# Optimization experiments

Hardware: AMD Instinct MI355X
Metric: run time of the kernel (lower is better)

Reference implementation:

```python
import jax, jax.numpy as jnp
import numpy as np


def setup_inputs() -> dict:
    key = jax.random.key(0)
    k1, k2, k3, k4 = jax.random.split(key, 4)
    B, N, d, E = 4, 768, 16, 12288
    emb_nodes = jax.random.normal(k1, (B, N, d), dtype=jnp.float32)
    edges = jax.random.randint(k2, (B, 2, E), 0, N, dtype=jnp.int64)
    # nn.Linear(2*d, 1): weight [1, 2d], bias [1]
    W = jax.random.normal(k3, (2 * d,), dtype=jnp.float32) * 0.1
    b = jax.random.normal(k4, (1,), dtype=jnp.float32) * 0.1
    return {"emb_nodes": emb_nodes, "edges": edges, "W": W, "b": b}


def reference(emb_nodes, edges, W, b):
    B, N, d = emb_nodes.shape
    # all-pairs (i, j): i = repeat_interleave, j = tile  -> [B, N*N, d]
    inter = jnp.repeat(emb_nodes, N, axis=1)
    rep = jnp.tile(emb_nodes, (1, N, 1))
    # original detaches the pair embeddings before the decoder
    edge_embeddings = jax.lax.stop_gradient(jnp.concatenate([inter, rep], axis=-1))  # [B, N*N, 2d]
    logits = edge_embeddings @ W + b[0]  # [B, N*N]
    # self-loop detection via embedding equality (|e_i - e_j| sum == 0)
    non_empty = jnp.abs(inter - rep).sum(axis=-1) != 0
    logits = jnp.where(non_empty, logits, jnp.float32(-10.0))
    # ground-truth edge indicator: scatter 1 at flat index i*N + j
    flat = edges[:, 0] * N + edges[:, 1]  # [B, E]
    truth = jnp.zeros((B, N * N), dtype=emb_nodes.dtype)
    truth = truth.at[jnp.arange(B)[:, None], flat].set(1.0)
    return (edge_embeddings, logits, truth)
```

## Files before the change

### kernel.cpp

```cpp
#include <hip/hip_runtime.h>

constexpr int B = 4;
constexpr int N = 768;
constexpr int D = 16;
constexpr int E = 12288;
constexpr int NN = N * N;
constexpr int PAIRS = B * NN;
constexpr long long EE_FLOATS = (long long)PAIRS * 2 * D;

__device__ __forceinline__ float dot4(float4 a, float4 b) {
    return a.x * b.x + a.y * b.y + a.z * b.z + a.w * b.w;
}
__device__ __forceinline__ float absdiff4(float4 a, float4 b) {
    return fabsf(a.x - b.x) + fabsf(a.y - b.y) + fabsf(a.z - b.z) + fabsf(a.w - b.w);
}

__global__ __launch_bounds__(256) void row_fused_kernel(
    const float4* __restrict__ emb4, const float* __restrict__ W,
    const float* __restrict__ bias, float4* __restrict__ ee4,
    float* __restrict__ logits, float* __restrict__ truth) {
    const int row = blockIdx.x;
    const int b = row / N;
    const int i = row - b * N;
    const float4* __restrict__ eb = emb4 + (size_t)b * N * 4;
    const float4* __restrict__ ei = eb + i * 4;

    const int t = threadIdx.x;
    const int q = t & 7;
    const int qq = q & 3;
    const bool isI = (q < 4);
    const float4 eiq = ei[qq];

    float4* __restrict__ orow = ee4 + (size_t)row * (N * 8);
#pragma unroll
    for (int k = 0; k < (N * 8) / 256; ++k) {
        const int f = t + k * 256;
        float4 v = eiq;
        if (!isI) v = eb[(f >> 3) * 4 + qq];
        orow[f] = v;
    }

    const float4* __restrict__ W4 = (const float4*)W;
    const float4 wa0 = W4[0], wa1 = W4[1], wa2 = W4[2], wa3 = W4[3];
    const float4 wb0 = W4[4], wb1 = W4[5], wb2 = W4[6], wb3 = W4[7];
    const float4 e0 = ei[0], e1 = ei[1], e2 = ei[2], e3 = ei[3];
    const float base =
        dot4(e0, wa0) + dot4(e1, wa1) + dot4(e2, wa2) + dot4(e3, wa3) + bias[0];
    float* __restrict__ lrow = logits + (size_t)row * N;
    float* __restrict__ trow = truth + (size_t)row * N;
#pragma unroll
    for (int k = 0; k < N / 256; ++k) {
        const int j = t + k * 256;
        const float4* __restrict__ ej = eb + j * 4;
        const float4 c0 = ej[0], c1 = ej[1], c2 = ej[2], c3 = ej[3];
        const float acc = base + dot4(c0, wb0) + dot4(c1, wb1) +
                          dot4(c2, wb2) + dot4(c3, wb3);
        const float diff = absdiff4(e0, c0) + absdiff4(e1, c1) +
                           absdiff4(e2, c2) + absdiff4(e3, c3);
        lrow[j] = (diff != 0.f) ? acc : -10.0f;
        trow[j] = 0.0f;
    }
}

__global__ void truth_scatter_kernel(const int* __restrict__ edges,
                                     float* __restrict__ truth) {
    int tid = blockIdx.x * blockDim.x + threadIdx.x;
    if (tid >= B * E) return;
    int b = tid / E;
    int e = tid - b * E;
    int src = edges[b * 2 * E + e];
    int dst = edges[b * 2 * E + E + e];
    truth[(size_t)b * NN + src * N + dst] = 1.0f;
}

extern "C" void kernel_launch(void* const* d_in, const int* in_sizes, int n_in,
                              void* d_out, int out_size, void* d_ws, size_t ws_size,
                              hipStream_t stream) {
    const float4* emb4 = (const float4*)d_in[0];
    const int* edges = (const int*)d_in[1];
    const float* W = (const float*)d_in[2];
    const float* bias = (const float*)d_in[3];

    float* out = (float*)d_out;
    float* ee = out;
    float* logits = out + EE_FLOATS;
    float* truth = out + EE_FLOATS + (long long)PAIRS;

    row_fused_kernel<<<B * N, 256, 0, stream>>>(emb4, W, bias, (float4*)ee,
                                                logits, truth);
    truth_scatter_kernel<<<(B * E + 255) / 256, 256, 0, stream>>>(edges, truth);
}
```

Measured before the change: 335.2 us.

## Stage node embeddings in LDS and process four rows per block with shuffle reductions

Each block now copies the batch's node embeddings into shared memory once and then handles four output rows instead of one. The logit and self-loop-difference sums are computed from the same float4 values being written to the edge-embedding output, using cross-lane shuffles, so the separate global reloads of each node are gone. This cuts redundant global and L2 reads and per-block setup. In exchange only one lane in eight writes logits and truth, those stores are strided, and the grid has four times fewer blocks. The kernel is dominated by output writes, so any gain is likely small.

```diff
diff --git a/kernel.cpp b/kernel.cpp
--- a/kernel.cpp
+++ b/kernel.cpp
@@ -7,6 +7,8 @@
 constexpr int NN = N * N;
 constexpr int PAIRS = B * NN;
 constexpr long long EE_FLOATS = (long long)PAIRS * 2 * D;
+constexpr int RPB = 4;
+constexpr int NQ = N * 4;
 
 __device__ __forceinline__ float dot4(float4 a, float4 b) {
     return a.x * b.x + a.y * b.y + a.z * b.z + a.w * b.w;
@@ -14,51 +16,74 @@
 __device__ __forceinline__ float absdiff4(float4 a, float4 b) {
     return fabsf(a.x - b.x) + fabsf(a.y - b.y) + fabsf(a.z - b.z) + fabsf(a.w - b.w);
 }
+__device__ __forceinline__ float4 sel4(int c, float4 a0, float4 a1, float4 a2, float4 a3) {
+    float4 r = a0;
+    if (c == 1) r = a1;
+    if (c == 2) r = a2;
+    if (c == 3) r = a3;
+    return r;
+}
 
-__global__ __launch_bounds__(256) void row_fused_kernel(
+__global__ __launch_bounds__(256) void rowgroup_fused_kernel(
     const float4* __restrict__ emb4, const float* __restrict__ W,
     const float* __restrict__ bias, float4* __restrict__ ee4,
     float* __restrict__ logits, float* __restrict__ truth) {
-    const int row = blockIdx.x;
-    const int b = row / N;
-    const int i = row - b * N;
-    const float4* __restrict__ eb = emb4 + (size_t)b * N * 4;
-    const float4* __restrict__ ei = eb + i * 4;
+    __shared__ float4 semb[NQ];
+
+    const int g = blockIdx.x;
+    const int b = g / (N / RPB);
+    const int i0 = (g - b * (N / RPB)) * RPB;
+    const float4* __restrict__ eb = emb4 + (size_t)b * NQ;
 
     const int t = threadIdx.x;
+#pragma unroll
+    for (int k = 0; k < NQ / 256; ++k)
+        semb[t + k * 256] = eb[t + k * 256];
+    __syncthreads();
+
     const int q = t & 7;
     const int qq = q & 3;
     const bool isI = (q < 4);
-    const float4 eiq = ei[qq];
-
-    float4* __restrict__ orow = ee4 + (size_t)row * (N * 8);
-#pragma unroll
-    for (int k = 0; k < (N * 8) / 256; ++k) {
-        const int f = t + k * 256;
-        float4 v = eiq;
-        if (!isI) v = eb[(f >> 3) * 4 + qq];
-        orow[f] = v;
-    }
+    const int jn0 = t >> 3;
+    const bool isWriter = (q == 4);
 
     const float4* __restrict__ W4 = (const float4*)W;
     const float4 wa0 = W4[0], wa1 = W4[1], wa2 = W4[2], wa3 = W4[3];
-    const float4 wb0 = W4[4], wb1 = W4[5], wb2 = W4[6], wb3 = W4[7];
-    const float4 e0 = ei[0], e1 = ei[1], e2 = ei[2], e3 = ei[3];
-    const float base =
-        dot4(e0, wa0) + dot4(e1, wa1) + dot4(e2, wa2) + dot4(e3, wa3) + bias[0];
-    float* __restrict__ lrow = logits + (size_t)row * N;
-    float* __restrict__ trow = truth + (size_t)row * N;
+    const float4 myWb = sel4(qq, W4[4], W4[5], W4[6], W4[7]);
+    const float bb = bias[0];
+
+#pragma unroll 1
+    for (int r = 0; r < RPB; ++r) {
+        const int i = i0 + r;
+        const int row = b * N + i;
+        const float4 e0 = semb[i * 4 + 0], e1 = semb[i * 4 + 1];
+        const float4 e2 = semb[i * 4 + 2], e3 = semb[i * 4 + 3];
+        const float base =
+            dot4(e0, wa0) + dot4(e1, wa1) + dot4(e2, wa2) + dot4(e3, wa3) + bb;
+        const float4 myEi = sel4(qq, e0, e1, e2, e3);
+
+        float4* __restrict__ orow = ee4 + (size_t)row * (N * 8);
+        float* __restrict__ lrow = logits + (size_t)row * N;
+        float* __restrict__ trow = truth + (size_t)row * N;
 #pragma unroll
-    for (int k = 0; k < N / 256; ++k) {
-        const int j = t + k * 256;
-        const float4* __restrict__ ej = eb + j * 4;
-        const float4 c0 = ej[0], c1 = ej[1], c2 = ej[2], c3 = ej[3];
-        const float acc = base + dot4(c0, wb0) + dot4(c1, wb1) +
-                          dot4(c2, wb2) + dot4(c3, wb3);
-        const float diff = absdiff4(e0, c0) + absdiff4(e1, c1) +
-                           absdiff4(e2, c2) + absdiff4(e3, c3);
-        lrow[j] = (diff != 0.f) ? acc : -10.0f;
-        trow[j] = 0.0f;
+        for (int k = 0; k < (N * 8) / 256; ++k) {
+            const int f = t + k * 256;
+            const int j = jn0 + k * 32;
+            const int node = isI ? i : j;
+            const float4 v = semb[node * 4 + qq];
+            orow[f] = v;
+
+            float pa = dot4(v, myWb);
+            float pd = absdiff4(myEi, v);
+            pa += __shfl_xor(pa, 1, 64);
+            pd += __shfl_xor(pd, 1, 64);
+            pa += __shfl_xor(pa, 2, 64);
+            pd += __shfl_xor(pd, 2, 64);
+            if (isWriter) {
+                lrow[j] = (pd != 0.f) ? (base + pa) : -10.0f;
+                trow[j] = 0.0f;
+            }
+        }
     }
 }
 
@@ -86,7 +111,7 @@
     float* logits = out + EE_FLOATS;
     float* truth = out + EE_FLOATS + (long long)PAIRS;
 
-    row_fused_kernel<<<B * N, 256, 0, stream>>>(emb4, W, bias, (float4*)ee,
-                                                logits, truth);
+    rowgroup_fused_kernel<<<B * N / RPB, 256, 0, stream>>>(
+        emb4, W, bias, (float4*)ee, logits, truth);
     truth_scatter_kernel<<<(B * E + 255) / 256, 256, 0, stream>>>(edges, truth);
 }
```

New measurement: 341.1 us. About the same (+1.8%).
